# Optimization experiments

Measured on AMD Instinct MI355X. Metric: run time of the kernel, lower is better.

The kernel has to match this reference:

```python
import jax, jax.numpy as jnp
import numpy as np
from jax import lax

K = 3      # kernel_size
PAD = 1    # padding (stride=1, dilation=1, groups=1 as in torchvision defaults)


def setup_inputs() -> dict:
    key = jax.random.key(0)
    ks = jax.random.split(key, 4)
    B, C, O, H, W = 4, 256, 256, 64, 64
    x = jax.random.normal(ks[0], (B, C, H, W), jnp.float32)
    # offset-predictor conv weights: small scale so predicted offsets are a few pixels
    w_off = jax.random.normal(ks[1], (2 * K * K, C, K, K), jnp.float32) * 0.01
    b_off = jnp.zeros((2 * K * K,), jnp.float32)
    # main deformable conv weights (kaiming-ish scale)
    w_def = jax.random.normal(ks[2], (O, C, K, K), jnp.float32) * (1.0 / np.sqrt(C * K * K))
    b_def = jnp.zeros((O,), jnp.float32)
    return {"x": x, "w_off": w_off, "b_off": b_off, "w_def": w_def, "b_def": b_def}


def _deform_conv(x, w_off, b_off, w_def, b_def):
    B, C, H, W = x.shape
    O = w_def.shape[0]
    KK = K * K
    # 1) predict offsets with a standard conv: [B, 2*K*K, H, W]
    offsets = lax.conv_general_dilated(x, w_off, (1, 1), [(PAD, PAD), (PAD, PAD)])
    offsets = offsets + b_off[None, :, None, None]
    # torchvision layout: channel 2*k is dy, 2*k+1 is dx for kernel tap k = ky*K+kx
    off = offsets.reshape(B, KK, 2, H, W)
    ky, kx = jnp.meshgrid(jnp.arange(K, dtype=jnp.float32),
                          jnp.arange(K, dtype=jnp.float32), indexing='ij')
    # sampling coords py/px: [B, KK, H, W]
    py = off[:, :, 0] + (jnp.arange(H, dtype=jnp.float32)[None, None, :, None]
                         + ky.reshape(-1)[None, :, None, None] - PAD)
    px = off[:, :, 1] + (jnp.arange(W, dtype=jnp.float32)[None, None, None, :]
                         + kx.reshape(-1)[None, :, None, None] - PAD)
    y0 = jnp.floor(py)
    x0 = jnp.floor(px)
    ly = py - y0
    lx = px - x0
    x_flat = x.reshape(B, C, H * W)
    gather = jax.vmap(lambda xf, ix: xf[:, ix])  # per-batch gather over spatial index
    sampled = jnp.zeros((B, C, KK, H, W), x.dtype)
    # bilinear interpolation with zero padding outside the image (4 corners)
    for dy_, wy in ((0.0, 1.0 - ly), (1.0, ly)):
        yi = y0 + dy_
        for dx_, wx in ((0.0, 1.0 - lx), (1.0, lx)):
            xi = x0 + dx_
            valid = (yi >= 0) & (yi < H) & (xi >= 0) & (xi < W)
            yc = jnp.clip(yi, 0, H - 1).astype(jnp.int32)
            xc = jnp.clip(xi, 0, W - 1).astype(jnp.int32)
            idx = (yc * W + xc).reshape(B, -1)               # [B, KK*H*W]
            vals = gather(x_flat, idx).reshape(B, C, KK, H, W)
            wgt = (wy * wx * valid).astype(x.dtype)          # [B, KK, H, W]
            sampled = sampled + vals * wgt[:, None]
    # 3) contract sampled patches with the deform-conv weight
    out = jnp.einsum('bckhw,ock->bohw', sampled, w_def.reshape(O, C, KK))
    return out + b_def[None, :, None, None]


def reference(x, w_off, b_off, w_def, b_def):
    return _deform_conv(x, w_off, b_off, w_def, b_def)
```

## Files before the change

kernel.cpp:

```cpp
#include <hip/hip_runtime.h>

#define B_ 4
#define C_ 256
#define O_ 256
#define H_ 64
#define W_ 64
#define HW 4096
#define NOFF 18
#define CK 2304

typedef __bf16 bf16x8 __attribute__((ext_vector_type(8)));
typedef float f32x4 __attribute__((ext_vector_type(4)));

__global__ __launch_bounds__(256) void wprep_def_kernel(
    const float* __restrict__ w_def, uint4* __restrict__ Wt4)
{
    __shared__ __bf16 wrow[CK];
    const int o = blockIdx.x;
    const int t = threadIdx.x;
#pragma unroll
    for (int q = 0; q < 9; ++q)
        wrow[t * 9 + q] = (__bf16)w_def[(size_t)o * CK + t * 9 + q];
    __syncthreads();
    for (int s = t; s < 288; s += 256) {
        const int ch = s >> 3, g = s & 7;
        const int kk = ch >> 2, cg = ch & 3;
        bf16x8 v;
#pragma unroll
        for (int j = 0; j < 8; ++j)
            v[j] = wrow[(cg * 64 + g * 8 + j) * 9 + kk];
        Wt4[(size_t)ch * 2048 + o * 8 + (g ^ (o & 7))] = __builtin_bit_cast(uint4, v);
    }
}

__global__ __launch_bounds__(256) void wprep_woff_kernel(
    const float* __restrict__ w_off, uint4* __restrict__ Woff4)
{
    const int ch = blockIdx.x;
    const int t = threadIdx.x;
    const int o = t >> 3, g = t & 7;
    const int kk = ch >> 2, cg = ch & 3;
    bf16x8 v;
#pragma unroll
    for (int j = 0; j < 8; ++j) {
        const int c = cg * 64 + g * 8 + j;
        v[j] = (o < NOFF) ? (__bf16)w_off[(size_t)o * CK + c * 9 + kk] : (__bf16)0.f;
    }
    Woff4[(size_t)ch * 256 + o * 8 + (g ^ (o & 7))] = __builtin_bit_cast(uint4, v);
}

__global__ __launch_bounds__(256, 4) void offs_mfma_kernel(
    const float* __restrict__ x, const uint4* __restrict__ Woff4,
    const float* __restrict__ b_off, float* __restrict__ offs)
{
    __shared__ float red[2][32][16];

    const int i = blockIdx.x;
    const int l = ((i & 7) << 6) + (i >> 3);
    const int ph = l & 1;
    const int bh = l >> 1;
    const int b = bh >> 6, h = bh & 63;

    const int t = threadIdx.x;
    const int w = t >> 6, lane = t & 63;
    const int l15 = lane & 15, l4 = lane >> 4;
    const int pxg = w & 1, kh = w >> 1;
    const int px = ph * 32 + pxg * 16 + l15;
    const float* xb = x + (size_t)b * C_ * HW;

    f32x4 acc0 = {0.f, 0.f, 0.f, 0.f}, acc1 = {0.f, 0.f, 0.f, 0.f};

    for (int kk = 0; kk < 9; ++kk) {
        const int ky = kk / 3, kx = kk - 3 * ky;
        const int y = h + ky - 1;
        const int col = px + kx - 1;
        const bool valid = (y >= 0) && (y < H_) && (col >= 0) && (col < W_);
#pragma unroll
        for (int cgl = 0; cgl < 2; ++cgl) {
            const int cg = kh * 2 + cgl;
            const int ch = kk * 4 + cg;
#pragma unroll
            for (int st = 0; st < 2; ++st) {
                const int g = st * 4 + l4;
                const int r0 = l15, r1 = 16 + l15;
                const bf16x8 a0 = __builtin_bit_cast(bf16x8,
                    Woff4[(size_t)ch * 256 + r0 * 8 + (g ^ (r0 & 7))]);
                const bf16x8 a1 = __builtin_bit_cast(bf16x8,
                    Woff4[(size_t)ch * 256 + r1 * 8 + (g ^ (r1 & 7))]);
                bf16x8 bF;
                if (valid) {
                    const float* p = xb + (size_t)(cg * 64 + g * 8) * HW + y * W_ + col;
#pragma unroll
                    for (int j = 0; j < 8; ++j)
                        bF[j] = (__bf16)p[(size_t)j * HW];
                } else {
#pragma unroll
                    for (int j = 0; j < 8; ++j) bF[j] = (__bf16)0.f;
                }
                acc0 = __builtin_amdgcn_mfma_f32_16x16x32_bf16(a0, bF, acc0, 0, 0, 0);
                acc1 = __builtin_amdgcn_mfma_f32_16x16x32_bf16(a1, bF, acc1, 0, 0, 0);
            }
        }
    }

    if (kh == 1) {
#pragma unroll
        for (int r = 0; r < 4; ++r) {
            red[pxg][l4 * 4 + r][l15] = acc0[r];
            red[pxg][16 + l4 * 4 + r][l15] = acc1[r];
        }
    }
    __syncthreads();
    if (kh == 0) {
#pragma unroll
        for (int ii = 0; ii < 2; ++ii) {
            const f32x4 a = ii ? acc1 : acc0;
#pragma unroll
            for (int r = 0; r < 4; ++r) {
                const int oc = ii * 16 + l4 * 4 + r;
                if (oc < NOFF) {
                    const float v = a[r] + red[pxg][oc][l15] + b_off[oc];
                    offs[((size_t)(bh * 64) + px) * NOFF + oc] = v;
                }
            }
        }
    }
}

__global__ __launch_bounds__(512, 4) void deform_mfma_kernel(
    const float* __restrict__ x, const float* __restrict__ offs,
    const uint4* __restrict__ Wt4, const float* __restrict__ b_def,
    float* __restrict__ out)
{
    __shared__ uint4 slab[4096];
    __shared__ uint4 Sl4[512];
    __shared__ float offs_lds[NOFF * 64];

    const int i = blockIdx.x;
    const int l = ((i & 7) << 6) + (i >> 3);
    const int oh = l & 1;
    const int bh = l >> 1;
    const int b = bh >> 6, h = bh & 63;
    const int obase = oh * 128;
    const int wb = h - 3;

    const int t = threadIdx.x;
    const int lane = t & 63;
    const int w = t >> 6;
    const int wo = w >> 1, wp = w & 1;
    const int l15 = lane & 15, l4 = lane >> 4;
    const int sp = t & 63;
    const int sg = w;
    const float* xb = x + (size_t)b * C_ * HW;

    auto stage_slab = [&](int cg) {
        const float* xc = xb + (size_t)(cg * 64 + sg * 8) * HW;
#pragma unroll
        for (int r = 0; r < 8; ++r) {
            const int yc = min(max(wb + r, 0), H_ - 1);
            bf16x8 v;
#pragma unroll
            for (int j = 0; j < 8; ++j)
                v[j] = (__bf16)xc[(size_t)j * HW + yc * W_ + sp];
            slab[(r * 64 + sp) * 8 + (sg ^ (sp & 7))] = __builtin_bit_cast(uint4, v);
        }
    };

    for (int idx = t; idx < NOFF * 64; idx += 512) {
        const int px = idx & 63, oc = idx >> 6;
        offs_lds[oc * 64 + px] = offs[((size_t)(bh * 64) + px) * NOFF + oc];
    }
    stage_slab(0);

    f32x4 acc[2][2];
#pragma unroll
    for (int ii = 0; ii < 2; ++ii)
#pragma unroll
        for (int j = 0; j < 2; ++j) acc[ii][j] = f32x4{0.f, 0.f, 0.f, 0.f};

    for (int cg = 0; cg < 4; ++cg) {
        if (cg != 0) stage_slab(cg);
        __syncthreads();
        const float* xsg = xb + (size_t)(cg * 64 + sg * 8) * HW;
        for (int kk = 0; kk < 9; ++kk) {
            const int ch = kk * 4 + cg;
            uint4 aR[2][2];
#pragma unroll
            for (int st = 0; st < 2; ++st) {
                const int g = st * 4 + l4;
#pragma unroll
                for (int ii = 0; ii < 2; ++ii) {
                    const int row = obase + wo * 32 + ii * 16 + l15;
                    aR[st][ii] = Wt4[(size_t)ch * 2048 + row * 8 + (g ^ (row & 7))];
                }
            }
            const int ky = kk / 3, kx = kk - 3 * ky;
            const float dy = offs_lds[(2 * kk) * 64 + sp];
            const float dx = offs_lds[(2 * kk + 1) * 64 + sp];
            const float py = (float)(h + ky - 1) + dy;
            const float pxf = (float)(sp + kx - 1) + dx;
            const float y0f = floorf(py), x0f = floorf(pxf);
            const float ly = py - y0f, lx = pxf - x0f;
            const int y0 = (int)y0f, x0 = (int)x0f;
            const int y1 = y0 + 1, x1 = x0 + 1;
            const bool vy0 = (y0 >= 0) && (y0 < H_), vy1 = (y1 >= 0) && (y1 < H_);
            const bool vx0 = (x0 >= 0) && (x0 < W_), vx1 = (x1 >= 0) && (x1 < W_);
            const float w00 = (vy0 && vx0) ? (1.f - ly) * (1.f - lx) : 0.f;
            const float w01 = (vy0 && vx1) ? (1.f - ly) * lx : 0.f;
            const float w10 = (vy1 && vx0) ? ly * (1.f - lx) : 0.f;
            const float w11 = (vy1 && vx1) ? ly * lx : 0.f;
            bf16x8 sv;
            if (y0 >= wb && y0 <= wb + 6) {
                const int s0 = y0 - wb;
                const int xc0 = min(max(x0, 0), W_ - 1);
                const int xc1 = min(max(x1, 0), W_ - 1);
                const int gx0 = sg ^ (xc0 & 7), gx1 = sg ^ (xc1 & 7);
                const bf16x8 c00 = __builtin_bit_cast(bf16x8, slab[(s0 * 64 + xc0) * 8 + gx0]);
                const bf16x8 c01 = __builtin_bit_cast(bf16x8, slab[(s0 * 64 + xc1) * 8 + gx1]);
                const bf16x8 c10 = __builtin_bit_cast(bf16x8, slab[((s0 + 1) * 64 + xc0) * 8 + gx0]);
                const bf16x8 c11 = __builtin_bit_cast(bf16x8, slab[((s0 + 1) * 64 + xc1) * 8 + gx1]);
#pragma unroll
                for (int j = 0; j < 8; ++j) {
                    const float v = w00 * (float)c00[j] + w01 * (float)c01[j]
                                  + w10 * (float)c10[j] + w11 * (float)c11[j];
                    sv[j] = (__bf16)v;
                }
            } else {
                const int y0c = min(max(y0, 0), H_ - 1), y1c = min(max(y1, 0), H_ - 1);
                const int xc0 = min(max(x0, 0), W_ - 1), xc1 = min(max(x1, 0), W_ - 1);
                const int i00 = y0c * W_ + xc0, i01 = y0c * W_ + xc1;
                const int i10 = y1c * W_ + xc0, i11 = y1c * W_ + xc1;
#pragma unroll
                for (int j = 0; j < 8; ++j) {
                    const float* p = xsg + (size_t)j * HW;
                    const float v = w00 * p[i00] + w01 * p[i01]
                                  + w10 * p[i10] + w11 * p[i11];
                    sv[j] = (__bf16)v;
                }
            }
            __syncthreads();
            Sl4[sp * 8 + (sg ^ (sp & 7))] = __builtin_bit_cast(uint4, sv);
            __syncthreads();
#pragma unroll
            for (int st = 0; st < 2; ++st) {
                const int g = st * 4 + l4;
                bf16x8 bF[2];
#pragma unroll
                for (int j = 0; j < 2; ++j) {
                    const int pr = wp * 32 + j * 16 + l15;
                    bF[j] = __builtin_bit_cast(bf16x8, Sl4[pr * 8 + (g ^ (pr & 7))]);
                }
#pragma unroll
                for (int ii = 0; ii < 2; ++ii)
#pragma unroll
                    for (int j = 0; j < 2; ++j)
                        acc[ii][j] = __builtin_amdgcn_mfma_f32_16x16x32_bf16(
                            __builtin_bit_cast(bf16x8, aR[st][ii]), bF[j],
                            acc[ii][j], 0, 0, 0);
            }
        }
        __syncthreads();
    }

#pragma unroll
    for (int ii = 0; ii < 2; ++ii) {
#pragma unroll
        for (int r = 0; r < 4; ++r) {
            const int o = obase + wo * 32 + ii * 16 + l4 * 4 + r;
            const float bias = b_def[o];
#pragma unroll
            for (int j = 0; j < 2; ++j) {
                const int p = wp * 32 + j * 16 + l15;
                out[(((size_t)(b * O_ + o)) * H_ + h) * W_ + p] = acc[ii][j][r] + bias;
            }
        }
    }
}

extern "C" void kernel_launch(void* const* d_in, const int* in_sizes, int n_in,
                              void* d_out, int out_size, void* d_ws, size_t ws_size,
                              hipStream_t stream) {
    const float* x     = (const float*)d_in[0];
    const float* w_off = (const float*)d_in[1];
    const float* b_off = (const float*)d_in[2];
    const float* w_def = (const float*)d_in[3];
    const float* b_def = (const float*)d_in[4];
    float* out = (float*)d_out;

    uint4* Wt4   = (uint4*)d_ws;
    uint4* Woff4 = Wt4 + 73728;
    float* offs  = (float*)(Woff4 + 9216);

    wprep_def_kernel<<<256, 256, 0, stream>>>(w_def, Wt4);
    wprep_woff_kernel<<<36, 256, 0, stream>>>(w_off, Woff4);
    offs_mfma_kernel<<<512, 256, 0, stream>>>(x, Woff4, b_off, offs);
    deform_mfma_kernel<<<512, 512, 0, stream>>>(x, offs, Wt4, b_def, out);
}
```

Measured before the change: 149.5 us.

## Split blocks by pixel half instead of output half to halve bilinear sampling work

Each block now covers all 256 output channels for 32 pixels, rather than 128 output channels for all 64 pixels. The bilinear sampling of each (pixel, channel, tap) is therefore done once instead of twice, by half of the threads. Offsets are loaded straight into registers instead of through LDS, and the sampled tile is double-buffered so one barrier per tap is removed. In exchange, half the threads sit idle during sampling, weight fragments are loaded across all 256 output channels, and the input slab is still staged per block, so slab loading work per output doubles.

```diff
diff --git a/kernel.cpp b/kernel.cpp
--- a/kernel.cpp
+++ b/kernel.cpp
@@ -133,28 +133,38 @@
     float* __restrict__ out)
 {
     __shared__ uint4 slab[4096];
-    __shared__ uint4 Sl4[512];
-    __shared__ float offs_lds[NOFF * 64];
+    __shared__ uint4 Sl4[2][256];
 
     const int i = blockIdx.x;
     const int l = ((i & 7) << 6) + (i >> 3);
-    const int oh = l & 1;
+    const int ph = l & 1;
     const int bh = l >> 1;
     const int b = bh >> 6, h = bh & 63;
-    const int obase = oh * 128;
     const int wb = h - 3;
 
     const int t = threadIdx.x;
     const int lane = t & 63;
     const int w = t >> 6;
-    const int wo = w >> 1, wp = w & 1;
     const int l15 = lane & 15, l4 = lane >> 4;
-    const int sp = t & 63;
-    const int sg = w;
+
+    const int sp = t & 63, sg8 = t >> 6;
+    const int pl = t & 31, sgs = (t >> 5) & 7;
+    const bool sampler = (t < 256);
+
     const float* xb = x + (size_t)b * C_ * HW;
 
+    float dyr[9], dxr[9];
+    if (sampler) {
+        const float* op = offs + ((size_t)(bh * 64) + ph * 32 + pl) * NOFF;
+#pragma unroll
+        for (int kk = 0; kk < 9; ++kk) {
+            const float2 d = *reinterpret_cast<const float2*>(op + 2 * kk);
+            dyr[kk] = d.x; dxr[kk] = d.y;
+        }
+    }
+
     auto stage_slab = [&](int cg) {
-        const float* xc = xb + (size_t)(cg * 64 + sg * 8) * HW;
+        const float* xc = xb + (size_t)(cg * 64 + sg8 * 8) * HW;
 #pragma unroll
         for (int r = 0; r < 8; ++r) {
             const int yc = min(max(wb + r, 0), H_ - 1);
@@ -162,16 +172,10 @@
 #pragma unroll
             for (int j = 0; j < 8; ++j)
                 v[j] = (__bf16)xc[(size_t)j * HW + yc * W_ + sp];
-            slab[(r * 64 + sp) * 8 + (sg ^ (sp & 7))] = __builtin_bit_cast(uint4, v);
+            slab[(r * 64 + sp) * 8 + (sg8 ^ (sp & 7))] = __builtin_bit_cast(uint4, v);
         }
     };
 
-    for (int idx = t; idx < NOFF * 64; idx += 512) {
-        const int px = idx & 63, oc = idx >> 6;
-        offs_lds[oc * 64 + px] = offs[((size_t)(bh * 64) + px) * NOFF + oc];
-    }
-    stage_slab(0);
-
     f32x4 acc[2][2];
 #pragma unroll
     for (int ii = 0; ii < 2; ++ii)
@@ -179,10 +183,13 @@
         for (int j = 0; j < 2; ++j) acc[ii][j] = f32x4{0.f, 0.f, 0.f, 0.f};
 
     for (int cg = 0; cg < 4; ++cg) {
-        if (cg != 0) stage_slab(cg);
+        if (cg != 0) __syncthreads();
+        stage_slab(cg);
         __syncthreads();
-        const float* xsg = xb + (size_t)(cg * 64 + sg * 8) * HW;
+        const float* xsg = xb + (size_t)(cg * 64 + sgs * 8) * HW;
+#pragma unroll
         for (int kk = 0; kk < 9; ++kk) {
+            const int buf = kk & 1;
             const int ch = kk * 4 + cg;
             uint4 aR[2][2];
 #pragma unroll
@@ -190,56 +197,55 @@
                 const int g = st * 4 + l4;
 #pragma unroll
                 for (int ii = 0; ii < 2; ++ii) {
-                    const int row = obase + wo * 32 + ii * 16 + l15;
+                    const int row = w * 32 + ii * 16 + l15;
                     aR[st][ii] = Wt4[(size_t)ch * 2048 + row * 8 + (g ^ (row & 7))];
                 }
             }
-            const int ky = kk / 3, kx = kk - 3 * ky;
-            const float dy = offs_lds[(2 * kk) * 64 + sp];
-            const float dx = offs_lds[(2 * kk + 1) * 64 + sp];
-            const float py = (float)(h + ky - 1) + dy;
-            const float pxf = (float)(sp + kx - 1) + dx;
-            const float y0f = floorf(py), x0f = floorf(pxf);
-            const float ly = py - y0f, lx = pxf - x0f;
-            const int y0 = (int)y0f, x0 = (int)x0f;
-            const int y1 = y0 + 1, x1 = x0 + 1;
-            const bool vy0 = (y0 >= 0) && (y0 < H_), vy1 = (y1 >= 0) && (y1 < H_);
-            const bool vx0 = (x0 >= 0) && (x0 < W_), vx1 = (x1 >= 0) && (x1 < W_);
-            const float w00 = (vy0 && vx0) ? (1.f - ly) * (1.f - lx) : 0.f;
-            const float w01 = (vy0 && vx1) ? (1.f - ly) * lx : 0.f;
-            const float w10 = (vy1 && vx0) ? ly * (1.f - lx) : 0.f;
-            const float w11 = (vy1 && vx1) ? ly * lx : 0.f;
-            bf16x8 sv;
-            if (y0 >= wb && y0 <= wb + 6) {
-                const int s0 = y0 - wb;
-                const int xc0 = min(max(x0, 0), W_ - 1);
-                const int xc1 = min(max(x1, 0), W_ - 1);
-                const int gx0 = sg ^ (xc0 & 7), gx1 = sg ^ (xc1 & 7);
-                const bf16x8 c00 = __builtin_bit_cast(bf16x8, slab[(s0 * 64 + xc0) * 8 + gx0]);
-                const bf16x8 c01 = __builtin_bit_cast(bf16x8, slab[(s0 * 64 + xc1) * 8 + gx1]);
-                const bf16x8 c10 = __builtin_bit_cast(bf16x8, slab[((s0 + 1) * 64 + xc0) * 8 + gx0]);
-                const bf16x8 c11 = __builtin_bit_cast(bf16x8, slab[((s0 + 1) * 64 + xc1) * 8 + gx1]);
-#pragma unroll
-                for (int j = 0; j < 8; ++j) {
-                    const float v = w00 * (float)c00[j] + w01 * (float)c01[j]
-                                  + w10 * (float)c10[j] + w11 * (float)c11[j];
-                    sv[j] = (__bf16)v;
-                }
-            } else {
-                const int y0c = min(max(y0, 0), H_ - 1), y1c = min(max(y1, 0), H_ - 1);
-                const int xc0 = min(max(x0, 0), W_ - 1), xc1 = min(max(x1, 0), W_ - 1);
-                const int i00 = y0c * W_ + xc0, i01 = y0c * W_ + xc1;
-                const int i10 = y1c * W_ + xc0, i11 = y1c * W_ + xc1;
-#pragma unroll
-                for (int j = 0; j < 8; ++j) {
-                    const float* p = xsg + (size_t)j * HW;
-                    const float v = w00 * p[i00] + w01 * p[i01]
-                                  + w10 * p[i10] + w11 * p[i11];
-                    sv[j] = (__bf16)v;
-                }
-            }
-            __syncthreads();
-            Sl4[sp * 8 + (sg ^ (sp & 7))] = __builtin_bit_cast(uint4, sv);
+            if (sampler) {
+                const int ky = kk / 3, kx = kk - 3 * ky;
+                const float py = (float)(h + ky - 1) + dyr[kk];
+                const float pxf = (float)(ph * 32 + pl + kx - 1) + dxr[kk];
+                const float y0f = floorf(py), x0f = floorf(pxf);
+                const float ly = py - y0f, lx = pxf - x0f;
+                const int y0 = (int)y0f, x0 = (int)x0f;
+                const int y1 = y0 + 1, x1 = x0 + 1;
+                const bool vy0 = (y0 >= 0) && (y0 < H_), vy1 = (y1 >= 0) && (y1 < H_);
+                const bool vx0 = (x0 >= 0) && (x0 < W_), vx1 = (x1 >= 0) && (x1 < W_);
+                const float w00 = (vy0 && vx0) ? (1.f - ly) * (1.f - lx) : 0.f;
+                const float w01 = (vy0 && vx1) ? (1.f - ly) * lx : 0.f;
+                const float w10 = (vy1 && vx0) ? ly * (1.f - lx) : 0.f;
+                const float w11 = (vy1 && vx1) ? ly * lx : 0.f;
+                bf16x8 sv;
+                if (y0 >= wb && y0 <= wb + 6) {
+                    const int s0 = y0 - wb;
+                    const int xc0 = min(max(x0, 0), W_ - 1);
+                    const int xc1 = min(max(x1, 0), W_ - 1);
+                    const int gx0 = sgs ^ (xc0 & 7), gx1 = sgs ^ (xc1 & 7);
+                    const bf16x8 c00 = __builtin_bit_cast(bf16x8, slab[(s0 * 64 + xc0) * 8 + gx0]);
+                    const bf16x8 c01 = __builtin_bit_cast(bf16x8, slab[(s0 * 64 + xc1) * 8 + gx1]);
+                    const bf16x8 c10 = __builtin_bit_cast(bf16x8, slab[((s0 + 1) * 64 + xc0) * 8 + gx0]);
+                    const bf16x8 c11 = __builtin_bit_cast(bf16x8, slab[((s0 + 1) * 64 + xc1) * 8 + gx1]);
+#pragma unroll
+                    for (int j = 0; j < 8; ++j) {
+                        const float v = w00 * (float)c00[j] + w01 * (float)c01[j]
+                                      + w10 * (float)c10[j] + w11 * (float)c11[j];
+                        sv[j] = (__bf16)v;
+                    }
+                } else {
+                    const int y0c = min(max(y0, 0), H_ - 1), y1c = min(max(y1, 0), H_ - 1);
+                    const int xc0 = min(max(x0, 0), W_ - 1), xc1 = min(max(x1, 0), W_ - 1);
+                    const int i00 = y0c * W_ + xc0, i01 = y0c * W_ + xc1;
+                    const int i10 = y1c * W_ + xc0, i11 = y1c * W_ + xc1;
+#pragma unroll
+                    for (int j = 0; j < 8; ++j) {
+                        const float* p = xsg + (size_t)j * HW;
+                        const float v = w00 * p[i00] + w01 * p[i01]
+                                      + w10 * p[i10] + w11 * p[i11];
+                        sv[j] = (__bf16)v;
+                    }
+                }
+                Sl4[buf][pl * 8 + (sgs ^ (pl & 7))] = __builtin_bit_cast(uint4, sv);
+            }
             __syncthreads();
 #pragma unroll
             for (int st = 0; st < 2; ++st) {
@@ -247,8 +253,8 @@
                 bf16x8 bF[2];
 #pragma unroll
                 for (int j = 0; j < 2; ++j) {
-                    const int pr = wp * 32 + j * 16 + l15;
-                    bF[j] = __builtin_bit_cast(bf16x8, Sl4[pr * 8 + (g ^ (pr & 7))]);
+                    const int pr = j * 16 + l15;
+                    bF[j] = __builtin_bit_cast(bf16x8, Sl4[buf][pr * 8 + (g ^ (pr & 7))]);
                 }
 #pragma unroll
                 for (int ii = 0; ii < 2; ++ii)
@@ -259,18 +265,17 @@
                             acc[ii][j], 0, 0, 0);
             }
         }
-        __syncthreads();
     }
 
 #pragma unroll
     for (int ii = 0; ii < 2; ++ii) {
 #pragma unroll
         for (int r = 0; r < 4; ++r) {
-            const int o = obase + wo * 32 + ii * 16 + l4 * 4 + r;
+            const int o = w * 32 + ii * 16 + l4 * 4 + r;
             const float bias = b_def[o];
 #pragma unroll
             for (int j = 0; j < 2; ++j) {
-                const int p = wp * 32 + j * 16 + l15;
+                const int p = ph * 32 + j * 16 + l15;
                 out[(((size_t)(b * O_ + o)) * H_ + h) * W_ + p] = acc[ii][j][r] + bias;
             }
         }
```

New measurement: 225.6 us. 1.51x slower.
